# Kernel tuning notes

Measured on AMD Instinct MI355X. Metric: run time of the kernel, lower is better.

Reference implementation:

```python
import jax, jax.numpy as jnp
import numpy as np

B, T, C = 4, 2048, 1024
NH, HS = 16, 64  # num_heads, head_size; NH*HS == C


def setup_inputs() -> dict:
    key = jax.random.key(0)
    ks = jax.random.split(key, 6)
    scale = C ** -0.5
    return {
        "x": jax.random.normal(ks[0], (B, T, C), dtype=jnp.float32),
        "Wk": jax.random.normal(ks[1], (C, C), dtype=jnp.float32) * scale,
        "Wq": jax.random.normal(ks[2], (C, C), dtype=jnp.float32) * scale,
        "Wv": jax.random.normal(ks[3], (C, C), dtype=jnp.float32) * scale,
        "Wp": jax.random.normal(ks[4], (C, C), dtype=jnp.float32) * scale,
        "bp": jax.random.normal(ks[5], (C,), dtype=jnp.float32) * 0.01,
    }


def reference(x, Wk, Wq, Wv, Wp, bp):
    # x: [B, T, C]. Linear(y) = y @ W.T (torch convention), no bias for k/q/v.
    def split_heads(t):
        return t.reshape(B, T, NH, HS).transpose(0, 2, 1, 3)  # [B, NH, T, HS]

    k = split_heads(x @ Wk.T)
    q = split_heads(x @ Wq.T)
    v = split_heads(x @ Wv.T)

    scores = jnp.einsum('bnqh,bnkh->bnqk', q, k) * (HS ** -0.5)  # [B,NH,T,T]
    causal = jnp.tril(jnp.ones((T, T), dtype=bool))
    scores = jnp.where(causal[None, None, :, :], scores, -jnp.inf)
    att = jax.nn.softmax(scores, axis=-1)
    out = jnp.einsum('bnqk,bnkh->bnqh', att, v)  # [B,NH,T,HS]
    out = out.transpose(0, 2, 1, 3).reshape(B, T, C)
    out = out @ Wp.T + bp
    return out
```

## Files before the change

kernel.cpp:

```cpp
#include <hip/hip_runtime.h>
#include <hip/hip_bf16.h>
#include <stdint.h>

typedef unsigned int uint;
typedef unsigned short ushort_t;
typedef unsigned long long ull;

#define B_ 4
#define T_ 2048
#define C_ 1024
#define NH_ 16
#define HS_ 64
#define M_ (B_*T_)
#define NBUF 6

typedef __bf16 bf16x8 __attribute__((ext_vector_type(8)));
typedef float f32x4 __attribute__((ext_vector_type(4)));

__device__ __forceinline__ ushort_t f2bf(float f) {
    uint u = __builtin_bit_cast(uint, f);
    u += 0x7fff + ((u >> 16) & 1);
    return (ushort_t)(u >> 16);
}

__device__ __forceinline__ void gload_lds16(const void* g, void* l) {
    __builtin_amdgcn_global_load_lds((const __attribute__((address_space(1))) void*)g,
                                     (__attribute__((address_space(3))) void*)l, 16, 0, 0);
}

__device__ __forceinline__ f32x4 mfma16(bf16x8 a, bf16x8 b, f32x4 c) {
    return __builtin_amdgcn_mfma_f32_16x16x32_bf16(a, b, c, 0, 0, 0);
}

__global__ void convert_bf16(const float* __restrict__ in, ushort_t* __restrict__ out,
                             int n4) {
    int i = blockIdx.x * blockDim.x + threadIdx.x;
    if (i >= n4) return;
    float4 v = ((const float4*)in)[i];
    ushort4 o;
    o.x = f2bf(v.x); o.y = f2bf(v.y); o.z = f2bf(v.z); o.w = f2bf(v.w);
    ((ushort4*)out)[i] = o;
}

__global__ void convert_w4(const float* __restrict__ Wq, const float* __restrict__ Wk,
                           const float* __restrict__ Wv, const float* __restrict__ Wp,
                           ushort_t* __restrict__ wqkv, ushort_t* __restrict__ wp) {
    int i = blockIdx.x * blockDim.x + threadIdx.x;
    int which = blockIdx.y;
    const float* src = (which == 0) ? Wq : (which == 1) ? Wk : (which == 2) ? Wv : Wp;
    ushort_t* dst = (which < 3) ? (wqkv + (size_t)which * C_ * C_) : wp;
    float scale = (which == 0) ? 0.125f * 1.44269504088896f : 1.0f;
    float4 v = ((const float4*)src)[i];
    ushort4 o;
    o.x = f2bf(v.x * scale); o.y = f2bf(v.y * scale);
    o.z = f2bf(v.z * scale); o.w = f2bf(v.w * scale);
    ((ushort4*)dst)[i] = o;
}

template<int MODE>
__global__ __launch_bounds__(512, 1) void gemm_nt(const ushort_t* __restrict__ A,
                                                  const ushort_t* __restrict__ Bw,
                                                  void* __restrict__ out0,
                                                  ushort_t* __restrict__ out1,
                                                  ushort_t* __restrict__ out2,
                                                  const float* __restrict__ bias) {
    __shared__ __align__(16) ushort_t As[NBUF][128 * 32];
    __shared__ __align__(16) ushort_t Bs[NBUF][256 * 32];

    const int tid  = threadIdx.x;
    const int lane = tid & 63;
    const int w    = tid >> 6;
    const int wm   = w >> 2;
    const int wn   = w & 3;
    const int r16  = lane & 15, g = lane >> 4;
    const int row0 = blockIdx.y * 128;
    const int col0 = blockIdx.x * 256;
    const int NK   = C_ / 32;

    f32x4 acc[4][4] = {};

    const int arow = tid >> 2, aj = tid & 3;
    const int ajs  = aj ^ ((arow & 3) ^ ((arow >> 2) & 3));
    const ushort_t* gA = A + (size_t)(row0 + arow) * C_ + ajs * 8;

    const int brow0 = tid >> 2,          bj0 = tid & 3;
    const int brow1 = (tid + 512) >> 2,  bj1 = tid & 3;
    const int bjs0  = bj0 ^ ((brow0 & 3) ^ ((brow0 >> 2) & 3));
    const int bjs1  = bj1 ^ ((brow1 & 3) ^ ((brow1 >> 2) & 3));
    const ushort_t* gB0 = Bw + (size_t)(col0 + brow0) * C_ + bjs0 * 8;
    const ushort_t* gB1 = Bw + (size_t)(col0 + brow1) * C_ + bjs1 * 8;

    auto stage = [&](int t, int b) {
        const int k0 = t * 32;
        gload_lds16(gA  + k0, &As[b][tid * 8]);
        gload_lds16(gB0 + k0, &Bs[b][tid * 8]);
        gload_lds16(gB1 + k0, &Bs[b][(tid + 512) * 8]);
    };

    auto compute = [&](int b) {
        const char* Ab = (const char*)&As[b][0];
        const char* Bb = (const char*)&Bs[b][0];
        bf16x8 af[4], bfv[4];
#pragma unroll
        for (int mf = 0; mf < 4; ++mf) {
            int row = wm * 64 + mf * 16 + r16;
            int sw  = g ^ ((row & 3) ^ ((row >> 2) & 3));
            af[mf] = *(const bf16x8*)(Ab + (row * 4 + sw) * 16);
        }
#pragma unroll
        for (int nf = 0; nf < 4; ++nf) {
            int row = wn * 64 + nf * 16 + r16;
            int sw  = g ^ ((row & 3) ^ ((row >> 2) & 3));
            bfv[nf] = *(const bf16x8*)(Bb + (row * 4 + sw) * 16);
        }
        __builtin_amdgcn_s_setprio(1);
#pragma unroll
        for (int mf = 0; mf < 4; ++mf)
#pragma unroll
            for (int nf = 0; nf < 4; ++nf)
                acc[mf][nf] = mfma16(af[mf], bfv[nf], acc[mf][nf]);
        __builtin_amdgcn_s_setprio(0);
    };

#pragma unroll
    for (int p = 0; p < 5; ++p) stage(p, p);

    int bcur = 0, bstg = 5, tstage = 5;

#define GSTEP(VMIMM) do {                                                    \
        __builtin_amdgcn_s_barrier();                                        \
        asm volatile("" ::: "memory");                                       \
        if (tstage < NK) {                                                   \
            stage(tstage, bstg);                                             \
            bstg = (bstg + 1 == NBUF) ? 0 : bstg + 1;                        \
        }                                                                    \
        ++tstage;                                                            \
        asm volatile("s_waitcnt vmcnt(" #VMIMM ")" ::: "memory");            \
        __builtin_amdgcn_s_barrier();                                        \
        asm volatile("" ::: "memory");                                       \
        compute(bcur);                                                       \
        bcur = (bcur + 1 == NBUF) ? 0 : bcur + 1;                            \
    } while (0)

    for (int t = 0; t < NK - 5; ++t) GSTEP(15);
    GSTEP(12); GSTEP(9); GSTEP(6); GSTEP(3); GSTEP(0);
#undef GSTEP

#pragma unroll
    for (int m = 0; m < 4; ++m) {
#pragma unroll
        for (int n = 0; n < 4; ++n) {
#pragma unroll
            for (int r = 0; r < 4; ++r) {
                int row = row0 + wm * 64 + m * 16 + g * 4 + r;
                int col = col0 + wn * 64 + n * 16 + r16;
                float val = acc[m][n][r];
                if (MODE == 2) {
                    ((float*)out0)[(size_t)row * C_ + col] = val + bias[col];
                } else {
                    int b = row >> 11, t = row & (T_ - 1);
                    int sect = col >> 10;
                    int c = col & (C_ - 1);
                    int h = c >> 6, hs = c & 63;
                    size_t bh = (size_t)(b * NH_ + h);
                    if (sect == 0)
                        ((ushort_t*)out0)[(bh * T_ + t) * HS_ + hs] = f2bf(val);
                    else if (sect == 1)
                        out1[(bh * T_ + t) * HS_ + hs] = f2bf(val);
                    else
                        out2[(bh * HS_ + hs) * T_ + t] = f2bf(val);
                }
            }
        }
    }
}

__global__ __launch_bounds__(512) void attn_fwd(const ushort_t* __restrict__ q,
                                                const ushort_t* __restrict__ k,
                                                const ushort_t* __restrict__ vT,
                                                ushort_t* __restrict__ o) {
    __shared__ __align__(16) ushort_t Kt[2][64 * 64];
    __shared__ __align__(16) ushort_t Vt[2][64 * 64];
    __shared__ __align__(16) ushort_t Pl[8][16 * 64];

    const int tid  = threadIdx.x;
    const int lane = tid & 63;
    const int w    = tid >> 6;
    const int r16  = lane & 15, g = lane >> 4;
    const int bid  = blockIdx.x;
    const int bh   = bid & 63;
    const int qt   = (T_ / 128 - 1) - (bid >> 6);
    const int qw   = qt * 128 + w * 16;
    const int nt   = 2 * qt + 2;

    const size_t hbase = (size_t)bh * T_ * HS_;

    bf16x8 qf[2];
#pragma unroll
    for (int s = 0; s < 2; ++s)
        qf[s] = *reinterpret_cast<const bf16x8*>(&q[hbase + (size_t)(qw + r16) * HS_ + s * 32 + g * 8]);

    f32x4 oacc[4] = {};
    float lrow[4] = {0.f, 0.f, 0.f, 0.f};

    {
        int s = tid, rr = s >> 3, j = s & 7, jg = j ^ (rr & 7);
        gload_lds16(k  + hbase + (size_t)rr * HS_ + jg * 8, &Kt[0][s * 8]);
        gload_lds16(vT + hbase + (size_t)rr * T_  + jg * 8, &Vt[0][s * 8]);
    }

    for (int kt = 0; kt < nt; ++kt) {
        const int cur = kt & 1;
        const int kb  = kt * 64;

        if (kt + 1 < nt) {
            int kb2 = kb + 64;
            int s = tid, rr = s >> 3, j = s & 7, jg = j ^ (rr & 7);
            gload_lds16(k  + hbase + (size_t)(kb2 + rr) * HS_ + jg * 8, &Kt[cur ^ 1][s * 8]);
            gload_lds16(vT + hbase + (size_t)rr * T_ + kb2 + jg * 8,    &Vt[cur ^ 1][s * 8]);
            asm volatile("s_waitcnt vmcnt(2)" ::: "memory");
        } else {
            asm volatile("s_waitcnt vmcnt(0)" ::: "memory");
        }
        __builtin_amdgcn_s_barrier();
        asm volatile("" ::: "memory");

        if (kb <= qw + 15) {
            f32x4 sacc[4] = {};
            __builtin_amdgcn_s_setprio(1);
#pragma unroll
            for (int n = 0; n < 4; ++n) {
#pragma unroll
                for (int s = 0; s < 2; ++s) {
                    int rowk = n * 16 + r16;
                    int cb = (s * 64 + g * 16) ^ ((rowk & 7) << 4);
                    bf16x8 kf = *reinterpret_cast<const bf16x8*>(
                        reinterpret_cast<const char*>(&Kt[cur][rowk * 64]) + cb);
                    sacc[n] = __builtin_amdgcn_mfma_f32_16x16x32_bf16(qf[s], kf, sacc[n], 0, 0, 0);
                }
            }
            __builtin_amdgcn_s_setprio(0);

            const bool need_mask = (kb + 63 > qw);
            ushort_t* pb = &Pl[w][0];
#pragma unroll
            for (int n = 0; n < 4; ++n) {
#pragma unroll
                for (int r = 0; r < 4; ++r) {
                    float sv = sacc[n][r];
                    if (need_mask) {
                        int kcol = kb + n * 16 + r16;
                        int qrow = qw + g * 4 + r;
                        if (kcol > qrow) sv = -1e30f;
                    }
                    float p = __builtin_amdgcn_exp2f(sv);
                    lrow[r] += p;
                    ushort_t pb16 = (ushort_t)((__builtin_bit_cast(uint, p) + 0x8000u) >> 16);
                    int prow = g * 4 + r;
                    int cb = (n * 32 + r16 * 2) ^ ((prow & 7) << 4);
                    *(ushort_t*)((char*)pb + prow * 128 + cb) = pb16;
                }
            }

            __builtin_amdgcn_s_setprio(1);
#pragma unroll
            for (int s = 0; s < 2; ++s) {
                int cbp = (s * 64 + g * 16) ^ ((r16 & 7) << 4);
                bf16x8 pf = *reinterpret_cast<const bf16x8*>((const char*)pb + r16 * 128 + cbp);
#pragma unroll
                for (int n = 0; n < 4; ++n) {
                    int rowv = n * 16 + r16;
                    int cbv = (s * 64 + g * 16) ^ ((rowv & 7) << 4);
                    bf16x8 vf = *reinterpret_cast<const bf16x8*>(
                        reinterpret_cast<const char*>(&Vt[cur][rowv * 64]) + cbv);
                    oacc[n] = __builtin_amdgcn_mfma_f32_16x16x32_bf16(pf, vf, oacc[n], 0, 0, 0);
                }
            }
            __builtin_amdgcn_s_setprio(0);
        }
        __builtin_amdgcn_s_barrier();
        asm volatile("" ::: "memory");
    }

#pragma unroll
    for (int mk = 1; mk <= 8; mk <<= 1)
#pragma unroll
        for (int r = 0; r < 4; ++r)
            lrow[r] += __shfl_xor(lrow[r], mk, 64);

    const int b = bh >> 4, h = bh & 15;
#pragma unroll
    for (int r = 0; r < 4; ++r) {
        float inv = 1.0f / lrow[r];
        int trow = qw + g * 4 + r;
        size_t obase = ((size_t)(b * T_ + trow) << 10) + h * 64;
#pragma unroll
        for (int n = 0; n < 4; ++n)
            o[obase + n * 16 + r16] = f2bf(oacc[n][r] * inv);
    }
}

extern "C" void kernel_launch(void* const* d_in, const int* in_sizes, int n_in,
                              void* d_out, int out_size, void* d_ws, size_t ws_size,
                              hipStream_t stream) {
    const float* x  = (const float*)d_in[0];
    const float* Wk = (const float*)d_in[1];
    const float* Wq = (const float*)d_in[2];
    const float* Wv = (const float*)d_in[3];
    const float* Wp = (const float*)d_in[4];
    const float* bp = (const float*)d_in[5];
    float* out = (float*)d_out;

    char* ws = (char*)d_ws;
    ushort_t* xbf  = (ushort_t*)(ws);
    ushort_t* wqkv = (ushort_t*)(ws + (size_t)(16 << 20));
    ushort_t* wpbf = (ushort_t*)(ws + (size_t)(22 << 20));
    ushort_t* qb   = (ushort_t*)(ws + (size_t)(24 << 20));
    ushort_t* kb   = (ushort_t*)(ws + (size_t)(40 << 20));
    ushort_t* vtb  = (ushort_t*)(ws + (size_t)(56 << 20));
    ushort_t* aob  = (ushort_t*)(ws + (size_t)(72 << 20));

    {
        int n4 = M_ * C_ / 4;
        convert_bf16<<<dim3((n4 + 255) / 256), dim3(256), 0, stream>>>(x, xbf, n4);
    }
    {
        int n4 = C_ * C_ / 4;
        convert_w4<<<dim3(n4 / 256, 4), dim3(256), 0, stream>>>(Wq, Wk, Wv, Wp, wqkv, wpbf);
    }

    gemm_nt<0><<<dim3(3 * C_ / 256, M_ / 128), 512, 0, stream>>>(xbf, wqkv, qb, kb, vtb, nullptr);

    attn_fwd<<<dim3((T_ / 128) * B_ * NH_), 512, 0, stream>>>(qb, kb, vtb, aob);

    gemm_nt<2><<<dim3(C_ / 256, M_ / 128), 512, 0, stream>>>(aob, wpbf, out, nullptr, nullptr, bp);
}
```

Measured before the change: 312.8 us.

## Shrink GEMM LDS ring to four buffers with single-barrier pipeline and new swizzle

Replaces the six-buffer, two-barrier-per-step load pipeline in the projection GEMM with a four-buffer ring that prefetches three tiles ahead and uses one barrier per k-step. It also changes the LDS XOR swizzle from a two-term row hash to (row>>1)&3. The aim is to cut barrier overhead and LDS footprint, at the cost of a shallower prefetch depth that may expose more global-load latency, and a different bank-conflict pattern.

New measurement: 304.2 us. 2.8% less time.

```diff
diff --git a/kernel.cpp b/kernel.cpp
--- a/kernel.cpp
+++ b/kernel.cpp
@@ -12,7 +12,6 @@
 #define NH_ 16
 #define HS_ 64
 #define M_ (B_*T_)
-#define NBUF 6
 
 typedef __bf16 bf16x8 __attribute__((ext_vector_type(8)));
 typedef float f32x4 __attribute__((ext_vector_type(4)));
@@ -64,8 +63,8 @@
                                                   ushort_t* __restrict__ out1,
                                                   ushort_t* __restrict__ out2,
                                                   const float* __restrict__ bias) {
-    __shared__ __align__(16) ushort_t As[NBUF][128 * 32];
-    __shared__ __align__(16) ushort_t Bs[NBUF][256 * 32];
+    __shared__ __align__(16) ushort_t As[4][128 * 32];
+    __shared__ __align__(16) ushort_t Bs[4][256 * 32];
 
     const int tid  = threadIdx.x;
     const int lane = tid & 63;
@@ -79,16 +78,16 @@
 
     f32x4 acc[4][4] = {};
 
-    const int arow = tid >> 2, aj = tid & 3;
-    const int ajs  = aj ^ ((arow & 3) ^ ((arow >> 2) & 3));
-    const ushort_t* gA = A + (size_t)(row0 + arow) * C_ + ajs * 8;
-
-    const int brow0 = tid >> 2,          bj0 = tid & 3;
-    const int brow1 = (tid + 512) >> 2,  bj1 = tid & 3;
-    const int bjs0  = bj0 ^ ((brow0 & 3) ^ ((brow0 >> 2) & 3));
-    const int bjs1  = bj1 ^ ((brow1 & 3) ^ ((brow1 >> 2) & 3));
-    const ushort_t* gB0 = Bw + (size_t)(col0 + brow0) * C_ + bjs0 * 8;
-    const ushort_t* gB1 = Bw + (size_t)(col0 + brow1) * C_ + bjs1 * 8;
+    const int ar  = tid >> 2;
+    const int aks = (tid & 3) ^ ((ar >> 1) & 3);
+    const ushort_t* gA  = A + (size_t)(row0 + ar) * C_ + aks * 8;
+
+    const int br0 = tid >> 2;
+    const int bk0 = (tid & 3) ^ ((br0 >> 1) & 3);
+    const int br1 = 128 + (tid >> 2);
+    const int bk1 = (tid & 3) ^ ((br1 >> 1) & 3);
+    const ushort_t* gB0 = Bw + (size_t)(col0 + br0) * C_ + bk0 * 8;
+    const ushort_t* gB1 = Bw + (size_t)(col0 + br1) * C_ + bk1 * 8;
 
     auto stage = [&](int t, int b) {
         const int k0 = t * 32;
@@ -97,21 +96,21 @@
         gload_lds16(gB1 + k0, &Bs[b][(tid + 512) * 8]);
     };
 
-    auto compute = [&](int b) {
+    auto tile_body = [&](int b) {
         const char* Ab = (const char*)&As[b][0];
         const char* Bb = (const char*)&Bs[b][0];
         bf16x8 af[4], bfv[4];
 #pragma unroll
         for (int mf = 0; mf < 4; ++mf) {
             int row = wm * 64 + mf * 16 + r16;
-            int sw  = g ^ ((row & 3) ^ ((row >> 2) & 3));
-            af[mf] = *(const bf16x8*)(Ab + (row * 4 + sw) * 16);
+            int js  = g ^ ((row >> 1) & 3);
+            af[mf] = *(const bf16x8*)(Ab + row * 64 + js * 16);
         }
 #pragma unroll
         for (int nf = 0; nf < 4; ++nf) {
             int row = wn * 64 + nf * 16 + r16;
-            int sw  = g ^ ((row & 3) ^ ((row >> 2) & 3));
-            bfv[nf] = *(const bf16x8*)(Bb + (row * 4 + sw) * 16);
+            int js  = g ^ ((row >> 1) & 3);
+            bfv[nf] = *(const bf16x8*)(Bb + row * 64 + js * 16);
         }
         __builtin_amdgcn_s_setprio(1);
 #pragma unroll
@@ -122,29 +121,23 @@
         __builtin_amdgcn_s_setprio(0);
     };
 
-#pragma unroll
-    for (int p = 0; p < 5; ++p) stage(p, p);
-
-    int bcur = 0, bstg = 5, tstage = 5;
-
-#define GSTEP(VMIMM) do {                                                    \
-        __builtin_amdgcn_s_barrier();                                        \
-        asm volatile("" ::: "memory");                                       \
-        if (tstage < NK) {                                                   \
-            stage(tstage, bstg);                                             \
-            bstg = (bstg + 1 == NBUF) ? 0 : bstg + 1;                        \
-        }                                                                    \
-        ++tstage;                                                            \
-        asm volatile("s_waitcnt vmcnt(" #VMIMM ")" ::: "memory");            \
-        __builtin_amdgcn_s_barrier();                                        \
-        asm volatile("" ::: "memory");                                       \
-        compute(bcur);                                                       \
-        bcur = (bcur + 1 == NBUF) ? 0 : bcur + 1;                            \
-    } while (0)
-
-    for (int t = 0; t < NK - 5; ++t) GSTEP(15);
-    GSTEP(12); GSTEP(9); GSTEP(6); GSTEP(3); GSTEP(0);
-#undef GSTEP
+    stage(0, 0); stage(1, 1); stage(2, 2);
+    int st = 3;
+
+#define WAITV(N) asm volatile("s_waitcnt vmcnt(" #N ")" ::: "memory")
+#define BARR()   do { __builtin_amdgcn_s_barrier(); asm volatile("" ::: "memory"); } while (0)
+
+    int t = 0;
+    for (; t < NK - 2; ++t) {
+        WAITV(6);
+        BARR();
+        if (st < NK) { stage(st, st & 3); ++st; }
+        tile_body(t & 3);
+    }
+    WAITV(3); BARR(); tile_body((NK - 2) & 3);
+    WAITV(0); BARR(); tile_body((NK - 1) & 3);
+#undef WAITV
+#undef BARR
 
 #pragma unroll
     for (int m = 0; m < 4; ++m) {
@@ -158,17 +151,17 @@
                 if (MODE == 2) {
                     ((float*)out0)[(size_t)row * C_ + col] = val + bias[col];
                 } else {
-                    int b = row >> 11, t = row & (T_ - 1);
+                    int b = row >> 11, tt = row & (T_ - 1);
                     int sect = col >> 10;
                     int c = col & (C_ - 1);
                     int h = c >> 6, hs = c & 63;
                     size_t bh = (size_t)(b * NH_ + h);
                     if (sect == 0)
-                        ((ushort_t*)out0)[(bh * T_ + t) * HS_ + hs] = f2bf(val);
+                        ((ushort_t*)out0)[(bh * T_ + tt) * HS_ + hs] = f2bf(val);
                     else if (sect == 1)
-                        out1[(bh * T_ + t) * HS_ + hs] = f2bf(val);
+                        out1[(bh * T_ + tt) * HS_ + hs] = f2bf(val);
                     else
-                        out2[(bh * HS_ + hs) * T_ + t] = f2bf(val);
+                        out2[(bh * HS_ + hs) * T_ + tt] = f2bf(val);
                 }
             }
         }
```
